# Kernel optimization log

Measured on AMD Instinct MI355X. Metric: run time of the kernel, lower is better.

The kernel has to match this reference:

```python
import jax, jax.numpy as jnp
import numpy as np
from jax import lax

B, N, D, H, K = 8, 1024, 384, 6, 7
HD = D // H
EPS = 1e-5


def layer_norm(x, g, b):
    m = jnp.mean(x, axis=-1, keepdims=True)
    v = jnp.mean(jnp.square(x - m), axis=-1, keepdims=True)
    return (x - m) * lax.rsqrt(v + EPS) * g + b


def setup_inputs() -> dict:
    key = jax.random.key(0)
    ks = jax.random.split(key, 12)
    s = 0.02
    return {
        "x": jax.random.normal(ks[0], (B, N, D), jnp.float32),
        "qkv_w": jax.random.normal(ks[1], (3 * D, D), jnp.float32) * s,
        "qkv_b": jnp.zeros((3 * D,), jnp.float32),
        "proj_w": jax.random.normal(ks[2], (D, D), jnp.float32) * s,
        "proj_b": jnp.zeros((D,), jnp.float32),
        "t_before": jnp.eye(H, dtype=jnp.float32) + jax.random.normal(ks[3], (H, H), jnp.float32) * 0.01,
        "t_after": jnp.eye(H, dtype=jnp.float32) + jax.random.normal(ks[4], (H, H), jnp.float32) * 0.01,
        "dw_w": jax.random.normal(ks[5], (D, 1, K), jnp.float32) * s,
        "dw_b": jnp.zeros((D,), jnp.float32),
        "mlp_ln_g": jnp.ones((D,), jnp.float32),
        "mlp_ln_b": jnp.zeros((D,), jnp.float32),
        "norm1_g": jnp.ones((D,), jnp.float32),
        "norm1_b": jnp.zeros((D,), jnp.float32),
        "norm2_g": jnp.ones((D,), jnp.float32),
        "norm2_b": jnp.zeros((D,), jnp.float32),
        "fc1_w": jax.random.normal(ks[6], (4 * D, D), jnp.float32) * s,
        "fc1_b": jnp.zeros((4 * D,), jnp.float32),
        "fc2_w": jax.random.normal(ks[7], (D, 4 * D), jnp.float32) * s,
        "fc2_b": jnp.zeros((D,), jnp.float32),
    }


def reference(x, qkv_w, qkv_b, proj_w, proj_b, t_before, t_after, dw_w, dw_b,
              mlp_ln_g, mlp_ln_b, norm1_g, norm1_b, norm2_g, norm2_b,
              fc1_w, fc1_b, fc2_w, fc2_b):
    # ---- attention branch ----
    h = layer_norm(x, norm1_g, norm1_b)
    qkv = h @ qkv_w.T + qkv_b                                  # (B,N,3D)
    qkv = qkv.reshape(B, N, 3, H, HD).transpose(2, 0, 3, 1, 4)  # (3,B,H,N,hd)
    q, k, v = qkv[0], qkv[1], qkv[2]
    scale = HD ** -0.5
    scores = jnp.einsum('bhnd,bhmd->bhnm', q, k) * scale        # (B,H,N,N)
    scores = jnp.einsum('gh,bhnm->bgnm', t_before, scores)       # head-mix pre-softmax
    probs = jax.nn.softmax(scores, axis=-1)
    probs = jnp.einsum('gh,bhnm->bgnm', t_after, probs)          # head-mix post-softmax
    attn_out = jnp.einsum('bhnm,bhmd->bhnd', probs, v)           # (B,H,N,hd)
    attn_out = attn_out.transpose(0, 2, 1, 3).reshape(B, N, D)
    attn_out = attn_out @ proj_w.T + proj_b
    x = x + attn_out
    # ---- MLP branch ----
    h = layer_norm(x, norm2_g, norm2_b)
    # depthwise conv1d over tokens: (B,D,N), groups=D, same padding
    h_t = h.transpose(0, 2, 1)
    h_t = lax.conv_general_dilated(h_t, dw_w, window_strides=(1,),
                                   padding=[(K // 2, K // 2)],
                                   dimension_numbers=('NCH', 'OIH', 'NCH'),
                                   feature_group_count=D)
    h = h_t.transpose(0, 2, 1) + dw_b
    h = layer_norm(h, mlp_ln_g, mlp_ln_b)
    h = jax.nn.gelu(h @ fc1_w.T + fc1_b, approximate=False)
    h = h @ fc2_w.T + fc2_b
    return x + h
```

## Files before the change

### kernel.cpp

```cpp
#include <hip/hip_runtime.h>
#include <hip/hip_bf16.h>

#define BB 8
#define NN 1024
#define DD 384
#define HH 6
#define HD 64
#define BN 8192
#define D3 1152
#define D4 1536
#define SEC 3145728

typedef __attribute__((ext_vector_type(8))) short short8;
typedef __attribute__((ext_vector_type(4))) float f32x4;

typedef __attribute__((address_space(3))) unsigned char as3_byte;
typedef __attribute__((address_space(1))) const unsigned char as1_byte;

__device__ __forceinline__ void gload16(const void* g, void* l){
  __builtin_amdgcn_global_load_lds((as1_byte*)g, (as3_byte*)l, 16, 0, 0);
}

__device__ __forceinline__ float b2f(unsigned short u){
  union{unsigned int i; float f;} x; x.i=((unsigned int)u)<<16; return x.f;
}
__device__ __forceinline__ unsigned short f2b(float f){
  unsigned int u=__float_as_uint(f);
  return (unsigned short)((u + 0x7FFFu + ((u>>16)&1u))>>16);
}

__global__ void cvt_kernel(const float* __restrict__ w0, const float* __restrict__ w1,
                           const float* __restrict__ w2, const float* __restrict__ w3,
                           unsigned short* __restrict__ out){
  int i = blockIdx.x*256 + threadIdx.x;
  float v;
  if (i < 442368)        v = w0[i];
  else if (i < 589824)   v = w1[i - 442368];
  else if (i < 1179648)  v = w2[i - 589824];
  else if (i < 1769472)  v = w3[i - 1179648];
  else return;
  out[i] = f2b(v);
}

template<int OUTBF>
__global__ __launch_bounds__(128)
void ln_kernel(const float* __restrict__ in, const float* __restrict__ gg, const float* __restrict__ bb,
               float* __restrict__ outf, unsigned short* __restrict__ outb){
  int row = blockIdx.x, t = threadIdx.x;
  const float* r = in + (size_t)row*DD;
  float v0=r[t], v1=r[t+128], v2=r[t+256];
  float s=v0+v1+v2, q=v0*v0+v1*v1+v2*v2;
  #pragma unroll
  for (int o=32;o>0;o>>=1){ s+=__shfl_down(s,o); q+=__shfl_down(q,o); }
  __shared__ float ls[2], lq[2];
  if ((t&63)==0){ ls[t>>6]=s; lq[t>>6]=q; }
  __syncthreads();
  float S=ls[0]+ls[1], Q=lq[0]+lq[1];
  float mean=S*(1.0f/DD);
  float rstd=rsqrtf(Q*(1.0f/DD)-mean*mean+1e-5f);
  float o0=(v0-mean)*rstd*gg[t]+bb[t];
  float o1=(v1-mean)*rstd*gg[t+128]+bb[t+128];
  float o2=(v2-mean)*rstd*gg[t+256]+bb[t+256];
  if (OUTBF){ unsigned short* o=outb+(size_t)row*DD; o[t]=f2b(o0); o[t+128]=f2b(o1); o[t+256]=f2b(o2); }
  else      { float* o=outf+(size_t)row*DD; o[t]=o0; o[t+128]=o1; o[t+256]=o2; }
}

__global__ __launch_bounds__(128)
void conv_ln_kernel(const float* __restrict__ h2, const float* __restrict__ dww, const float* __restrict__ dwb,
                    const float* __restrict__ gg, const float* __restrict__ bb, unsigned short* __restrict__ out){
  int row=blockIdx.x, t=threadIdx.x;
  int bi=row>>10, n=row&1023;
  const float* base = h2 + (size_t)(bi<<10)*DD;
  float a[3];
  #pragma unroll
  for (int j=0;j<3;j++){
    int d=t+j*128;
    float acc=dwb[d];
    #pragma unroll
    for (int k=0;k<7;k++){
      int nn=n+k-3;
      if (nn>=0 && nn<NN) acc += dww[d*7+k]*base[(size_t)nn*DD + d];
    }
    a[j]=acc;
  }
  float s=a[0]+a[1]+a[2], q=a[0]*a[0]+a[1]*a[1]+a[2]*a[2];
  #pragma unroll
  for (int o=32;o>0;o>>=1){ s+=__shfl_down(s,o); q+=__shfl_down(q,o); }
  __shared__ float ls[2], lq[2];
  if ((t&63)==0){ ls[t>>6]=s; lq[t>>6]=q; }
  __syncthreads();
  float S=ls[0]+ls[1], Q=lq[0]+lq[1];
  float mean=S*(1.0f/DD);
  float rstd=rsqrtf(Q*(1.0f/DD)-mean*mean+1e-5f);
  unsigned short* o = out + (size_t)row*DD;
  #pragma unroll
  for (int j=0;j<3;j++){
    int d=t+j*128;
    o[d]=f2b((a[j]-mean)*rstd*gg[d]+bb[d]);
  }
}

template<int MODE, int TN>
__global__ __launch_bounds__(256)
void gemm_kernel(const unsigned short* __restrict__ A, const unsigned short* __restrict__ W,
                 const float* __restrict__ bias, const float* __restrict__ resid,
                 float* __restrict__ outf, unsigned short* __restrict__ outb,
                 int Kdim, int Ncols){
  constexpr int JF = TN/32;
  __shared__ __align__(16) unsigned short lds_a[128*32];
  __shared__ __align__(16) unsigned short lds_b[TN*32];
  int t=threadIdx.x, lane=t&63, w=t>>6;
  int bm = blockIdx.x*128;
  int bn = blockIdx.y*TN;
  int wr = w>>1, wc = w&1;
  int rm = lane&15, r16 = lane>>4;
  f32x4 acc[4][JF] = {};
  char* ldsa_c = (char*)lds_a;
  char* ldsb_c = (char*)lds_b;
  int abyte[4], bbyte[JF];
  #pragma unroll
  for (int i=0;i<4;i++){
    int ra = wr*64 + i*16 + rm;
    abyte[i] = ra*64 + ((r16 ^ ((ra>>1)&3))*16);
  }
  #pragma unroll
  for (int j=0;j<JF;j++){
    int rb = wc*(TN/2) + j*16 + rm;
    bbyte[j] = rb*64 + ((r16 ^ ((rb>>1)&3))*16);
  }
  int niter = Kdim>>5;
  for (int it=0; it<niter; ++it){
    int k0 = it<<5;
    if (it) __syncthreads();
    #pragma unroll
    for (int c=0;c<2;c++){
      int u = t + c*256;
      int row = u>>2, sl = (u&3) ^ ((row>>1)&3);
      gload16(A + (size_t)(bm+row)*Kdim + k0 + sl*8, ldsa_c + u*16);
    }
    #pragma unroll
    for (int c=0;c<TN/64;c++){
      int u = t + c*256;
      int row = u>>2, sl = (u&3) ^ ((row>>1)&3);
      gload16(W + (size_t)(bn+row)*Kdim + k0 + sl*8, ldsb_c + u*16);
    }
    __syncthreads();
    short8 af[4], bf[JF];
    #pragma unroll
    for (int i=0;i<4;i++) af[i]=*reinterpret_cast<const short8*>(ldsa_c + abyte[i]);
    #pragma unroll
    for (int j=0;j<JF;j++) bf[j]=*reinterpret_cast<const short8*>(ldsb_c + bbyte[j]);
    #pragma unroll
    for (int i=0;i<4;i++)
      #pragma unroll
      for (int j=0;j<JF;j++)
        acc[i][j]=__builtin_amdgcn_mfma_f32_16x16x32_bf16(af[i],bf[j],acc[i][j],0,0,0);
  }
  #pragma unroll
  for (int i=0;i<4;i++){
    #pragma unroll
    for (int j=0;j<JF;j++){
      #pragma unroll
      for (int r=0;r<4;r++){
        int row = bm + wr*64 + i*16 + r16*4 + r;
        int col = bn + wc*(TN/2) + j*16 + rm;
        float v = acc[i][j][r] + bias[col];
        if (MODE==0){
          int c = col/384; int rem = col - c*384; int hh = rem>>6, d = rem&63;
          if (c==0) v *= 0.125f;
          int bi = row>>10, nn = row&1023;
          outb[(size_t)c*SEC + (((size_t)(bi*6+hh))<<16) + (nn<<6) + d] = f2b(v);
        } else if (MODE==1){
          size_t idx = (size_t)row*Ncols + col;
          outf[idx] = resid[idx] + v;
        } else {
          float ge = 0.5f*v*(1.0f+erff(v*0.70710678118654752f));
          outb[(size_t)row*Ncols + col] = f2b(ge);
        }
      }
    }
  }
}

__global__ __launch_bounds__(256)
void vt8_kernel(const unsigned short* __restrict__ V, unsigned char* __restrict__ V8){
  __shared__ unsigned short tile[64][66];
  int z = blockIdx.y, m0 = blockIdx.x*64;
  int t = threadIdx.x, c = t&63, r4 = t>>6;
  #pragma unroll
  for (int p=0;p<16;p++){
    int m = r4 + p*4;
    tile[m][c] = V[((size_t)z<<16) + ((size_t)(m0+m)<<6) + c];
  }
  __syncthreads();
  #pragma unroll
  for (int p=0;p<16;p++){
    int d = r4 + p*4;
    float v = b2f(tile[c][d]);
    int pk = __builtin_amdgcn_cvt_pk_fp8_f32(v, v, 0, false);
    V8[((size_t)z<<16) + ((size_t)d<<10) + m0 + c] = (unsigned char)(pk & 0xff);
  }
}

__global__ __launch_bounds__(512)
void smx_kernel(const unsigned short* __restrict__ qkv,
                const float* __restrict__ tbm, const float* __restrict__ tam,
                unsigned char* __restrict__ P){
  __shared__ __align__(16) unsigned short Qs[6*32*64];
  __shared__ __align__(16) unsigned short Ks[6*64*64];
  __shared__ __align__(16) unsigned char  Pt[6*32*68];
  __shared__ float lred[8][6][16];
  int t=threadIdx.x, lane=t&63, w=t>>6;
  int b = blockIdx.x&7, nt = blockIdx.x>>3;
  int n0 = nt*32;
  int nh = w>>2, mq = (w&3)*16;
  int c16 = lane&15, r16 = lane>>4;
  #pragma unroll
  for (int i=0;i<3;i++){
    int u = t + i*512;
    int r = u>>3, s = u&7;
    int h = r>>5, n = r&31;
    gload16(qkv + (((size_t)(b*6+h))<<16) + ((size_t)(n0+n)<<6) + ((s ^ (r&7))*8),
            (char*)Qs + u*16);
  }
  float tbr[36], tar[36];
  #pragma unroll
  for (int i=0;i<36;i++){ tbr[i]=tbm[i]; tar[i]=tam[i]; }
  __syncthreads();
  short8 qf[6][2];
  #pragma unroll
  for (int h=0;h<6;h++){
    int r = h*32 + nh*16 + c16;
    #pragma unroll
    for (int kk=0;kk<2;kk++)
      qf[h][kk] = *(const short8*)((char*)Qs + r*128 + (((kk*4+r16) ^ (r&7))<<4));
  }
  float lsum[6] = {0.f,0.f,0.f,0.f,0.f,0.f};
  float invl[6] = {0.f,0.f,0.f,0.f,0.f,0.f};
  const unsigned short* kbase = qkv + SEC + (((size_t)(b*6))<<16);
  for (int pass=0; pass<2; ++pass){
    for (int mt=0; mt<16; ++mt){
      int m0 = mt*64;
      __syncthreads();
      #pragma unroll
      for (int i=0;i<6;i++){
        int u = t + i*512;
        int r = u>>3, s = u&7;
        int h = r>>6, m = r&63;
        gload16(kbase + (((size_t)h)<<16) + ((size_t)(m0+m)<<6) + ((s ^ (r&7))*8),
                (char*)Ks + u*16);
      }
      __syncthreads();
      f32x4 aq[6] = {};
      #pragma unroll
      for (int h=0;h<6;h++){
        #pragma unroll
        for (int kk=0;kk<2;kk++){
          int r = h*64 + mq + c16;
          short8 kf = *(const short8*)((char*)Ks + r*128 + (((kk*4+r16) ^ (r&7))<<4));
          aq[h] = __builtin_amdgcn_mfma_f32_16x16x32_bf16(kf, qf[h][kk], aq[h], 0,0,0);
        }
      }
      if (pass==0){
        #pragma unroll
        for (int r=0;r<4;r++){
          float s0=aq[0][r], s1=aq[1][r], s2=aq[2][r],
                s3=aq[3][r], s4=aq[4][r], s5=aq[5][r];
          #pragma unroll
          for (int g=0;g<6;g++){
            float sm = tbr[g*6]*s0 + tbr[g*6+1]*s1 + tbr[g*6+2]*s2
                     + tbr[g*6+3]*s3 + tbr[g*6+4]*s4 + tbr[g*6+5]*s5;
            lsum[g] += __expf(sm);
          }
        }
      } else {
        float pf[6][4];
        #pragma unroll
        for (int r=0;r<4;r++){
          float s0=aq[0][r], s1=aq[1][r], s2=aq[2][r],
                s3=aq[3][r], s4=aq[4][r], s5=aq[5][r];
          float e[6];
          #pragma unroll
          for (int g=0;g<6;g++){
            float sm = tbr[g*6]*s0 + tbr[g*6+1]*s1 + tbr[g*6+2]*s2
                     + tbr[g*6+3]*s3 + tbr[g*6+4]*s4 + tbr[g*6+5]*s5;
            e[g] = __expf(sm) * invl[g];
          }
          #pragma unroll
          for (int g2=0;g2<6;g2++)
            pf[g2][r] = tar[g2*6]*e[0] + tar[g2*6+1]*e[1] + tar[g2*6+2]*e[2]
                      + tar[g2*6+3]*e[3] + tar[g2*6+4]*e[4] + tar[g2*6+5]*e[5];
        }
        #pragma unroll
        for (int g2=0;g2<6;g2++){
          int pkv = __builtin_amdgcn_cvt_pk_fp8_f32(pf[g2][0], pf[g2][1], 0, false);
          pkv = __builtin_amdgcn_cvt_pk_fp8_f32(pf[g2][2], pf[g2][3], pkv, true);
          *(int*)(Pt + (g2*32 + nh*16 + c16)*68 + mq + r16*4) = pkv;
        }
        __syncthreads();
        #pragma unroll
        for (int i=0;i<6;i++){
          int u = t + i*512;
          int row = u>>4, col = u&15;
          int g = row>>5, n = row&31;
          unsigned int dv = *(const unsigned int*)(Pt + row*68 + col*4);
          *(unsigned int*)(P + (((size_t)(b*6+g))<<20) + ((size_t)(n0+n)<<10) + m0 + col*4) = dv;
        }
      }
    }
    if (pass==0){
      #pragma unroll
      for (int g=0;g<6;g++){
        lsum[g] += __shfl_xor(lsum[g],16);
        lsum[g] += __shfl_xor(lsum[g],32);
      }
      if (r16==0){
        #pragma unroll
        for (int g=0;g<6;g++) lred[w][g][c16] = lsum[g];
      }
      __syncthreads();
      #pragma unroll
      for (int g=0;g<6;g++)
        invl[g] = 256.0f/(lred[nh*4][g][c16]+lred[nh*4+1][g][c16]
                         +lred[nh*4+2][g][c16]+lred[nh*4+3][g][c16]);
    }
  }
}

__global__ __launch_bounds__(256)
void pv8_gemm(const unsigned char* __restrict__ P, const unsigned char* __restrict__ V8,
              unsigned short* __restrict__ outp){
  __shared__ __align__(16) unsigned char As[64*64];
  __shared__ __align__(16) unsigned char Bs[64*64];
  int t=threadIdx.x, lane=t&63, w=t>>6;
  int z = blockIdx.y;
  int bn = blockIdx.x*64;
  int wr = w>>1, wc = w&1;
  int c16=lane&15, r16=lane>>4;
  f32x4 acc[2][2] = {};
  const unsigned char* Pz = P + ((size_t)z<<20);
  const unsigned char* Vz = V8 + ((size_t)z<<16);
  int arow = t>>2, aslot = (t&3) ^ (arow&3);
  int abyte[2], bbyte2[2];
  #pragma unroll
  for (int i=0;i<2;i++){
    int ra = wr*32 + i*16 + c16;
    abyte[i] = ra*64 + ((r16&1)<<3);
    int rb = wc*32 + i*16 + c16;
    bbyte2[i] = rb*64 + ((r16&1)<<3);
  }
  for (int mt=0; mt<16; ++mt){
    int m0 = mt*64;
    if (mt) __syncthreads();
    gload16(Pz + ((size_t)(bn+arow)<<10) + m0 + aslot*16, (char*)As + t*16);
    gload16(Vz + ((size_t)arow<<10) + m0 + aslot*16, (char*)Bs + t*16);
    __syncthreads();
    #pragma unroll
    for (int kk=0;kk<2;kk++){
      long afr[2], bfr[2];
      #pragma unroll
      for (int i=0;i<2;i++){
        int ra = wr*32 + i*16 + c16;
        int sa = (kk*2 + (r16>>1)) ^ (ra&3);
        afr[i] = *(const long*)((char*)As + abyte[i] + (sa<<4) - ((abyte[i]>>4)&0)*0 - ( ( (r16&1)<<3 ) - ((r16&1)<<3) ));
        afr[i] = *(const long*)((char*)As + ra*64 + (sa<<4) + ((r16&1)<<3));
        int rb = wc*32 + i*16 + c16;
        int sb = (kk*2 + (r16>>1)) ^ (rb&3);
        bfr[i] = *(const long*)((char*)Bs + rb*64 + (sb<<4) + ((r16&1)<<3));
      }
      #pragma unroll
      for (int i=0;i<2;i++)
        #pragma unroll
        for (int j=0;j<2;j++)
          acc[i][j] = __builtin_amdgcn_mfma_f32_16x16x32_fp8_fp8(afr[i], bfr[j], acc[i][j], 0,0,0);
    }
  }
  int bl = z/6, g = z - bl*6;
  #pragma unroll
  for (int i=0;i<2;i++)
    #pragma unroll
    for (int j=0;j<2;j++)
      #pragma unroll
      for (int r=0;r<4;r++){
        int n = bn + wr*32 + i*16 + r16*4 + r;
        int d = wc*32 + j*16 + c16;
        outp[((size_t)((bl<<10)|n))*DD + g*64 + d] = f2b(acc[i][j][r] * 0.00390625f);
      }
}

extern "C" void kernel_launch(void* const* d_in, const int* in_sizes, int n_in,
                              void* d_out, int out_size, void* d_ws, size_t ws_size,
                              hipStream_t stream){
  const float* x      = (const float*)d_in[0];
  const float* qkv_w  = (const float*)d_in[1];
  const float* qkv_b  = (const float*)d_in[2];
  const float* proj_w = (const float*)d_in[3];
  const float* proj_b = (const float*)d_in[4];
  const float* t_before=(const float*)d_in[5];
  const float* t_after =(const float*)d_in[6];
  const float* dw_w   = (const float*)d_in[7];
  const float* dw_b   = (const float*)d_in[8];
  const float* mlp_g  = (const float*)d_in[9];
  const float* mlp_b  = (const float*)d_in[10];
  const float* n1_g   = (const float*)d_in[11];
  const float* n1_b   = (const float*)d_in[12];
  const float* n2_g   = (const float*)d_in[13];
  const float* n2_b   = (const float*)d_in[14];
  const float* fc1_w  = (const float*)d_in[15];
  const float* fc1_b  = (const float*)d_in[16];
  const float* fc2_w  = (const float*)d_in[17];
  const float* fc2_b  = (const float*)d_in[18];
  float* out = (float*)d_out;
  char* ws = (char*)d_ws;
  unsigned short* qkvwb = (unsigned short*)(ws + 0);
  unsigned short* projwb= (unsigned short*)(ws + 884736);
  unsigned short* fc1wb = (unsigned short*)(ws + 1179648);
  unsigned short* fc2wb = (unsigned short*)(ws + 2359296);
  unsigned short* hb    = (unsigned short*)(ws + 3538944);
  unsigned short* qkvb  = (unsigned short*)(ws + 9830400);
  unsigned char*  V8    = (unsigned char*) (ws + 28704768);
  unsigned char*  Pp    = (unsigned char*) (ws + 34996224);
  unsigned short* attnb = (unsigned short*)(ws + 85327872);
  float*          x2    = (float*)(ws + 91619328);
  float* h2 = (float*)qkvb;
  unsigned short* hcln = hb;
  unsigned short* fc1o = (unsigned short*)Pp;

  cvt_kernel<<<(1769472+255)/256,256,0,stream>>>(qkv_w, proj_w, fc1_w, fc2_w, qkvwb);

  ln_kernel<1><<<BN,128,0,stream>>>(x, n1_g, n1_b, nullptr, hb);
  { dim3 g(BN/128, D3/128); gemm_kernel<0,128><<<g,256,0,stream>>>(hb, qkvwb, qkv_b, nullptr, nullptr, qkvb, DD, D3); }
  { dim3 g(NN/64, 48); vt8_kernel<<<g,256,0,stream>>>(qkvb + 2*(size_t)SEC, V8); }
  smx_kernel<<<256,512,0,stream>>>(qkvb, t_before, t_after, Pp);
  { dim3 g(16, 48); pv8_gemm<<<g,256,0,stream>>>(Pp, V8, attnb); }
  { dim3 g(BN/128, DD/64); gemm_kernel<1,64><<<g,256,0,stream>>>(attnb, projwb, proj_b, x, x2, nullptr, DD, DD); }
  ln_kernel<0><<<BN,128,0,stream>>>(x2, n2_g, n2_b, h2, nullptr);
  conv_ln_kernel<<<BN,128,0,stream>>>(h2, dw_w, dw_b, mlp_g, mlp_b, hcln);
  { dim3 g(BN/128, D4/128); gemm_kernel<2,128><<<g,256,0,stream>>>(hcln, fc1wb, fc1_b, nullptr, nullptr, fc1o, DD, D4); }
  { dim3 g(BN/128, DD/64); gemm_kernel<1,64><<<g,256,0,stream>>>(fc1o, fc2wb, fc2_b, x2, out, nullptr, D4, DD); }
}
```

Measured before the change: 221.7 us.

## Double-buffer LDS tiles in GEMM, softmax and PV kernels; use exp2

Adds two-stage LDS double buffering to the bf16 GEMM, the two-pass head-mixed softmax kernel and the fp8 PV GEMM, so the next tile's global-to-LDS load is issued before computing on the current one, with a single barrier per iteration. The softmax kernel also folds log2(e) into the pre-softmax mixing matrix to use the hardware exp2, and writes fp8 probabilities straight to global memory instead of going through an LDS transpose tile. This doubles LDS footprint, which can lower occupancy, especially in the softmax kernel with 96KB of K buffers. The direct P stores are also narrower per-thread writes than the previous coalesced layout.

```diff
diff --git a/kernel.cpp b/kernel.cpp
--- a/kernel.cpp
+++ b/kernel.cpp
@@ -107,8 +107,8 @@
                  float* __restrict__ outf, unsigned short* __restrict__ outb,
                  int Kdim, int Ncols){
   constexpr int JF = TN/32;
-  __shared__ __align__(16) unsigned short lds_a[128*32];
-  __shared__ __align__(16) unsigned short lds_b[TN*32];
+  __shared__ __align__(16) unsigned short lds_a[2][128*32];
+  __shared__ __align__(16) unsigned short lds_b[2][TN*32];
   int t=threadIdx.x, lane=t&63, w=t>>6;
   int bm = blockIdx.x*128;
   int bn = blockIdx.y*TN;
@@ -128,33 +128,37 @@
     int rb = wc*(TN/2) + j*16 + rm;
     bbyte[j] = rb*64 + ((r16 ^ ((rb>>1)&3))*16);
   }
-  int niter = Kdim>>5;
-  for (int it=0; it<niter; ++it){
-    int k0 = it<<5;
-    if (it) __syncthreads();
+  auto stage = [&](int buf, int k0){
     #pragma unroll
     for (int c=0;c<2;c++){
       int u = t + c*256;
       int row = u>>2, sl = (u&3) ^ ((row>>1)&3);
-      gload16(A + (size_t)(bm+row)*Kdim + k0 + sl*8, ldsa_c + u*16);
+      gload16(A + (size_t)(bm+row)*Kdim + k0 + sl*8, ldsa_c + buf*8192 + u*16);
     }
     #pragma unroll
     for (int c=0;c<TN/64;c++){
       int u = t + c*256;
       int row = u>>2, sl = (u&3) ^ ((row>>1)&3);
-      gload16(W + (size_t)(bn+row)*Kdim + k0 + sl*8, ldsb_c + u*16);
-    }
-    __syncthreads();
+      gload16(W + (size_t)(bn+row)*Kdim + k0 + sl*8, ldsb_c + buf*(TN*64) + u*16);
+    }
+  };
+  int niter = Kdim>>5;
+  stage(0, 0);
+  __syncthreads();
+  for (int it=0; it<niter; ++it){
+    if (it+1<niter) stage((it+1)&1, (it+1)<<5);
+    int ab = (it&1)*8192, bb2 = (it&1)*(TN*64);
     short8 af[4], bf[JF];
     #pragma unroll
-    for (int i=0;i<4;i++) af[i]=*reinterpret_cast<const short8*>(ldsa_c + abyte[i]);
-    #pragma unroll
-    for (int j=0;j<JF;j++) bf[j]=*reinterpret_cast<const short8*>(ldsb_c + bbyte[j]);
+    for (int i=0;i<4;i++) af[i]=*reinterpret_cast<const short8*>(ldsa_c + ab + abyte[i]);
+    #pragma unroll
+    for (int j=0;j<JF;j++) bf[j]=*reinterpret_cast<const short8*>(ldsb_c + bb2 + bbyte[j]);
     #pragma unroll
     for (int i=0;i<4;i++)
       #pragma unroll
       for (int j=0;j<JF;j++)
         acc[i][j]=__builtin_amdgcn_mfma_f32_16x16x32_bf16(af[i],bf[j],acc[i][j],0,0,0);
+    __syncthreads();
   }
   #pragma unroll
   for (int i=0;i<4;i++){
@@ -207,14 +211,24 @@
                 const float* __restrict__ tbm, const float* __restrict__ tam,
                 unsigned char* __restrict__ P){
   __shared__ __align__(16) unsigned short Qs[6*32*64];
-  __shared__ __align__(16) unsigned short Ks[6*64*64];
-  __shared__ __align__(16) unsigned char  Pt[6*32*68];
+  __shared__ __align__(16) unsigned short Ks[2][6*64*64];
   __shared__ float lred[8][6][16];
   int t=threadIdx.x, lane=t&63, w=t>>6;
   int b = blockIdx.x&7, nt = blockIdx.x>>3;
   int n0 = nt*32;
   int nh = w>>2, mq = (w&3)*16;
   int c16 = lane&15, r16 = lane>>4;
+  const unsigned short* kbase = qkv + SEC + (((size_t)(b*6))<<16);
+  auto stageK = [&](int buf, int m0){
+    #pragma unroll
+    for (int i=0;i<6;i++){
+      int u = t + i*512;
+      int r = u>>3, s = u&7;
+      int h = r>>6, m = r&63;
+      gload16(kbase + (((size_t)h)<<16) + ((size_t)(m0+m)<<6) + ((s ^ (r&7))*8),
+              (char*)Ks + buf*49152 + u*16);
+    }
+  };
   #pragma unroll
   for (int i=0;i<3;i++){
     int u = t + i*512;
@@ -223,9 +237,10 @@
     gload16(qkv + (((size_t)(b*6+h))<<16) + ((size_t)(n0+n)<<6) + ((s ^ (r&7))*8),
             (char*)Qs + u*16);
   }
+  stageK(0, 0);
   float tbr[36], tar[36];
   #pragma unroll
-  for (int i=0;i<36;i++){ tbr[i]=tbm[i]; tar[i]=tam[i]; }
+  for (int i=0;i<36;i++){ tbr[i]=tbm[i]*1.44269504088896f; tar[i]=tam[i]; }
   __syncthreads();
   short8 qf[6][2];
   #pragma unroll
@@ -236,102 +251,96 @@
       qf[h][kk] = *(const short8*)((char*)Qs + r*128 + (((kk*4+r16) ^ (r&7))<<4));
   }
   float lsum[6] = {0.f,0.f,0.f,0.f,0.f,0.f};
-  float invl[6] = {0.f,0.f,0.f,0.f,0.f,0.f};
-  const unsigned short* kbase = qkv + SEC + (((size_t)(b*6))<<16);
-  for (int pass=0; pass<2; ++pass){
-    for (int mt=0; mt<16; ++mt){
-      int m0 = mt*64;
-      __syncthreads();
-      #pragma unroll
-      for (int i=0;i<6;i++){
-        int u = t + i*512;
-        int r = u>>3, s = u&7;
-        int h = r>>6, m = r&63;
-        gload16(kbase + (((size_t)h)<<16) + ((size_t)(m0+m)<<6) + ((s ^ (r&7))*8),
-                (char*)Ks + u*16);
-      }
-      __syncthreads();
-      f32x4 aq[6] = {};
-      #pragma unroll
-      for (int h=0;h<6;h++){
-        #pragma unroll
-        for (int kk=0;kk<2;kk++){
-          int r = h*64 + mq + c16;
-          short8 kf = *(const short8*)((char*)Ks + r*128 + (((kk*4+r16) ^ (r&7))<<4));
-          aq[h] = __builtin_amdgcn_mfma_f32_16x16x32_bf16(kf, qf[h][kk], aq[h], 0,0,0);
-        }
-      }
-      if (pass==0){
-        #pragma unroll
-        for (int r=0;r<4;r++){
-          float s0=aq[0][r], s1=aq[1][r], s2=aq[2][r],
-                s3=aq[3][r], s4=aq[4][r], s5=aq[5][r];
-          #pragma unroll
-          for (int g=0;g<6;g++){
-            float sm = tbr[g*6]*s0 + tbr[g*6+1]*s1 + tbr[g*6+2]*s2
-                     + tbr[g*6+3]*s3 + tbr[g*6+4]*s4 + tbr[g*6+5]*s5;
-            lsum[g] += __expf(sm);
-          }
-        }
-      } else {
-        float pf[6][4];
-        #pragma unroll
-        for (int r=0;r<4;r++){
-          float s0=aq[0][r], s1=aq[1][r], s2=aq[2][r],
-                s3=aq[3][r], s4=aq[4][r], s5=aq[5][r];
-          float e[6];
-          #pragma unroll
-          for (int g=0;g<6;g++){
-            float sm = tbr[g*6]*s0 + tbr[g*6+1]*s1 + tbr[g*6+2]*s2
-                     + tbr[g*6+3]*s3 + tbr[g*6+4]*s4 + tbr[g*6+5]*s5;
-            e[g] = __expf(sm) * invl[g];
-          }
-          #pragma unroll
-          for (int g2=0;g2<6;g2++)
-            pf[g2][r] = tar[g2*6]*e[0] + tar[g2*6+1]*e[1] + tar[g2*6+2]*e[2]
-                      + tar[g2*6+3]*e[3] + tar[g2*6+4]*e[4] + tar[g2*6+5]*e[5];
-        }
-        #pragma unroll
-        for (int g2=0;g2<6;g2++){
-          int pkv = __builtin_amdgcn_cvt_pk_fp8_f32(pf[g2][0], pf[g2][1], 0, false);
-          pkv = __builtin_amdgcn_cvt_pk_fp8_f32(pf[g2][2], pf[g2][3], pkv, true);
-          *(int*)(Pt + (g2*32 + nh*16 + c16)*68 + mq + r16*4) = pkv;
-        }
-        __syncthreads();
-        #pragma unroll
-        for (int i=0;i<6;i++){
-          int u = t + i*512;
-          int row = u>>4, col = u&15;
-          int g = row>>5, n = row&31;
-          unsigned int dv = *(const unsigned int*)(Pt + row*68 + col*4);
-          *(unsigned int*)(P + (((size_t)(b*6+g))<<20) + ((size_t)(n0+n)<<10) + m0 + col*4) = dv;
-        }
-      }
-    }
-    if (pass==0){
+  float invl[6];
+  for (int mt=0; mt<16; ++mt){
+    if (mt<15) stageK((mt+1)&1, (mt+1)*64);
+    else       stageK(0, 0);
+    int kb = (mt&1)*49152;
+    f32x4 aq[6] = {};
+    #pragma unroll
+    for (int h=0;h<6;h++){
+      #pragma unroll
+      for (int kk=0;kk<2;kk++){
+        int r = h*64 + mq + c16;
+        short8 kf = *(const short8*)((char*)Ks + kb + r*128 + (((kk*4+r16) ^ (r&7))<<4));
+        aq[h] = __builtin_amdgcn_mfma_f32_16x16x32_bf16(kf, qf[h][kk], aq[h], 0,0,0);
+      }
+    }
+    #pragma unroll
+    for (int r=0;r<4;r++){
+      float s0=aq[0][r], s1=aq[1][r], s2=aq[2][r],
+            s3=aq[3][r], s4=aq[4][r], s5=aq[5][r];
       #pragma unroll
       for (int g=0;g<6;g++){
-        lsum[g] += __shfl_xor(lsum[g],16);
-        lsum[g] += __shfl_xor(lsum[g],32);
-      }
-      if (r16==0){
-        #pragma unroll
-        for (int g=0;g<6;g++) lred[w][g][c16] = lsum[g];
-      }
-      __syncthreads();
-      #pragma unroll
-      for (int g=0;g<6;g++)
-        invl[g] = 256.0f/(lred[nh*4][g][c16]+lred[nh*4+1][g][c16]
-                         +lred[nh*4+2][g][c16]+lred[nh*4+3][g][c16]);
-    }
+        float sm = tbr[g*6]*s0 + tbr[g*6+1]*s1 + tbr[g*6+2]*s2
+                 + tbr[g*6+3]*s3 + tbr[g*6+4]*s4 + tbr[g*6+5]*s5;
+        lsum[g] += __builtin_amdgcn_exp2f(sm);
+      }
+    }
+    __syncthreads();
+  }
+  #pragma unroll
+  for (int g=0;g<6;g++){
+    lsum[g] += __shfl_xor(lsum[g],16);
+    lsum[g] += __shfl_xor(lsum[g],32);
+  }
+  if (r16==0){
+    #pragma unroll
+    for (int g=0;g<6;g++) lred[w][g][c16] = lsum[g];
+  }
+  __syncthreads();
+  #pragma unroll
+  for (int g=0;g<6;g++)
+    invl[g] = 256.0f/(lred[nh*4][g][c16]+lred[nh*4+1][g][c16]
+                     +lred[nh*4+2][g][c16]+lred[nh*4+3][g][c16]);
+  int nrow = n0 + nh*16 + c16;
+  for (int mt=0; mt<16; ++mt){
+    int m0 = mt*64;
+    if (mt<15) stageK((mt+1)&1, (mt+1)*64);
+    int kb = (mt&1)*49152;
+    f32x4 aq[6] = {};
+    #pragma unroll
+    for (int h=0;h<6;h++){
+      #pragma unroll
+      for (int kk=0;kk<2;kk++){
+        int r = h*64 + mq + c16;
+        short8 kf = *(const short8*)((char*)Ks + kb + r*128 + (((kk*4+r16) ^ (r&7))<<4));
+        aq[h] = __builtin_amdgcn_mfma_f32_16x16x32_bf16(kf, qf[h][kk], aq[h], 0,0,0);
+      }
+    }
+    float pf[6][4];
+    #pragma unroll
+    for (int r=0;r<4;r++){
+      float s0=aq[0][r], s1=aq[1][r], s2=aq[2][r],
+            s3=aq[3][r], s4=aq[4][r], s5=aq[5][r];
+      float e[6];
+      #pragma unroll
+      for (int g=0;g<6;g++){
+        float sm = tbr[g*6]*s0 + tbr[g*6+1]*s1 + tbr[g*6+2]*s2
+                 + tbr[g*6+3]*s3 + tbr[g*6+4]*s4 + tbr[g*6+5]*s5;
+        e[g] = __builtin_amdgcn_exp2f(sm) * invl[g];
+      }
+      #pragma unroll
+      for (int g2=0;g2<6;g2++)
+        pf[g2][r] = tar[g2*6]*e[0] + tar[g2*6+1]*e[1] + tar[g2*6+2]*e[2]
+                  + tar[g2*6+3]*e[3] + tar[g2*6+4]*e[4] + tar[g2*6+5]*e[5];
+    }
+    #pragma unroll
+    for (int g2=0;g2<6;g2++){
+      int pkv = __builtin_amdgcn_cvt_pk_fp8_f32(pf[g2][0], pf[g2][1], 0, false);
+      pkv = __builtin_amdgcn_cvt_pk_fp8_f32(pf[g2][2], pf[g2][3], pkv, true);
+      *(unsigned int*)(P + (((size_t)(b*6+g2))<<20) + ((size_t)nrow<<10) + m0 + mq + r16*4)
+        = (unsigned int)pkv;
+    }
+    __syncthreads();
   }
 }
 
 __global__ __launch_bounds__(256)
 void pv8_gemm(const unsigned char* __restrict__ P, const unsigned char* __restrict__ V8,
               unsigned short* __restrict__ outp){
-  __shared__ __align__(16) unsigned char As[64*64];
-  __shared__ __align__(16) unsigned char Bs[64*64];
+  __shared__ __align__(16) unsigned char As[2][64*64];
+  __shared__ __align__(16) unsigned char Bs[2][64*64];
   int t=threadIdx.x, lane=t&63, w=t>>6;
   int z = blockIdx.y;
   int bn = blockIdx.x*64;
@@ -341,20 +350,15 @@
   const unsigned char* Pz = P + ((size_t)z<<20);
   const unsigned char* Vz = V8 + ((size_t)z<<16);
   int arow = t>>2, aslot = (t&3) ^ (arow&3);
-  int abyte[2], bbyte2[2];
-  #pragma unroll
-  for (int i=0;i<2;i++){
-    int ra = wr*32 + i*16 + c16;
-    abyte[i] = ra*64 + ((r16&1)<<3);
-    int rb = wc*32 + i*16 + c16;
-    bbyte2[i] = rb*64 + ((r16&1)<<3);
-  }
+  auto stage = [&](int buf, int m0){
+    gload16(Pz + ((size_t)(bn+arow)<<10) + m0 + aslot*16, (char*)As + buf*4096 + t*16);
+    gload16(Vz + ((size_t)arow<<10) + m0 + aslot*16, (char*)Bs + buf*4096 + t*16);
+  };
+  stage(0, 0);
+  __syncthreads();
   for (int mt=0; mt<16; ++mt){
-    int m0 = mt*64;
-    if (mt) __syncthreads();
-    gload16(Pz + ((size_t)(bn+arow)<<10) + m0 + aslot*16, (char*)As + t*16);
-    gload16(Vz + ((size_t)arow<<10) + m0 + aslot*16, (char*)Bs + t*16);
-    __syncthreads();
+    if (mt+1<16) stage((mt+1)&1, (mt+1)*64);
+    int off = (mt&1)*4096;
     #pragma unroll
     for (int kk=0;kk<2;kk++){
       long afr[2], bfr[2];
@@ -362,11 +366,10 @@
       for (int i=0;i<2;i++){
         int ra = wr*32 + i*16 + c16;
         int sa = (kk*2 + (r16>>1)) ^ (ra&3);
-        afr[i] = *(const long*)((char*)As + abyte[i] + (sa<<4) - ((abyte[i]>>4)&0)*0 - ( ( (r16&1)<<3 ) - ((r16&1)<<3) ));
-        afr[i] = *(const long*)((char*)As + ra*64 + (sa<<4) + ((r16&1)<<3));
+        afr[i] = *(const long*)((char*)As + off + ra*64 + (sa<<4) + ((r16&1)<<3));
         int rb = wc*32 + i*16 + c16;
         int sb = (kk*2 + (r16>>1)) ^ (rb&3);
-        bfr[i] = *(const long*)((char*)Bs + rb*64 + (sb<<4) + ((r16&1)<<3));
+        bfr[i] = *(const long*)((char*)Bs + off + rb*64 + (sb<<4) + ((r16&1)<<3));
       }
       #pragma unroll
       for (int i=0;i<2;i++)
@@ -374,6 +377,7 @@
         for (int j=0;j<2;j++)
           acc[i][j] = __builtin_amdgcn_mfma_f32_16x16x32_fp8_fp8(afr[i], bfr[j], acc[i][j], 0,0,0);
     }
+    __syncthreads();
   }
   int bl = z/6, g = z - bl*6;
   #pragma unroll
```

Result: faster. 211.9 us (-4.4%).
